# Performance work log

Hardware: AMD Instinct MI355X
Metric: run time of the kernel (lower is better)

## Reference

```python
import jax, jax.numpy as jnp
import numpy as np

D_MODEL = 1024
D_INNER = 2048  # d_model * expand_factor
EPS = 1e-6


def setup_inputs() -> dict:
    key = jax.random.key(0)
    ks = jax.random.split(key, 9)
    s_in = 1.0 / np.sqrt(D_MODEL)
    s_out = 1.0 / np.sqrt(D_INNER)
    x = jax.random.normal(ks[0], (4, 2048, D_MODEL), dtype=jnp.float32)
    # weights stored as [in, out] (transpose of nn.Linear layout)
    Wq = jax.random.uniform(ks[1], (D_MODEL, D_INNER), jnp.float32, -s_in, s_in)
    bq = jax.random.uniform(ks[2], (D_INNER,), jnp.float32, -s_in, s_in)
    Wk = jax.random.uniform(ks[3], (D_MODEL, D_INNER), jnp.float32, -s_in, s_in)
    bk = jax.random.uniform(ks[4], (D_INNER,), jnp.float32, -s_in, s_in)
    Wv = jax.random.uniform(ks[5], (D_MODEL, D_INNER), jnp.float32, -s_in, s_in)
    bv = jax.random.uniform(ks[6], (D_INNER,), jnp.float32, -s_in, s_in)
    Wo = jax.random.uniform(ks[7], (D_INNER, D_MODEL), jnp.float32, -s_out, s_out)
    bo = jax.random.uniform(ks[8], (D_MODEL,), jnp.float32, -s_out, s_out)
    return {"x": x, "Wq": Wq, "bq": bq, "Wk": Wk, "bk": bk,
            "Wv": Wv, "bv": bv, "Wo": Wo, "bo": bo}


def _phi(x):
    """ELU + 1 feature map (positive features)."""
    return jax.nn.elu(x) + 1.0


def reference(x, Wq, bq, Wk, bk, Wv, bv, Wo, bo):
    # x: [B, N, d_model]
    Q = _phi(x @ Wq + bq)          # [B, N, d_inner]
    K = _phi(x @ Wk + bk)          # [B, N, d_inner]
    V = x @ Wv + bv                # [B, N, d_inner]
    n = x.shape[1]
    # Causal linear attention; identical math to cumsum-of-outer-products:
    # numerator_n = sum_{m<=n} (Q_n . K_m) V_m ; denominator_n = sum_{m<=n} Q_n . K_m
    scores = jnp.einsum("bnd,bmd->bnm", Q, K)            # [B, N, N]
    mask = jnp.tril(jnp.ones((n, n), dtype=scores.dtype))
    scores = scores * mask
    numerator = jnp.einsum("bnm,bme->bne", scores, V)    # [B, N, d_inner]
    denominator = scores.sum(axis=-1, keepdims=True) + EPS
    out = numerator / denominator
    return out @ Wo + bo           # [B, N, d_model] (dropout is identity in eval)
```

## Files before the change

kernel.cpp:

```cpp
#include <hip/hip_runtime.h>
#include <hip/hip_bf16.h>


#define D_MODEL 1024
#define D_INNER 2048
#define SEQ     2048
#define NBATCH  4
#define MTOT    (NBATCH * SEQ)

typedef __attribute__((ext_vector_type(8))) __bf16 bf16x8;
typedef __attribute__((ext_vector_type(4))) float  f32x4;
typedef __attribute__((ext_vector_type(8))) short  short8v;
typedef __attribute__((ext_vector_type(4))) int    int4v;
typedef __attribute__((ext_vector_type(8))) int    int8v;

__device__ __forceinline__ short f2bf(float f) {
  union { float f; unsigned u; } x; x.f = f;
  unsigned r = x.u + 0x7fffu + ((x.u >> 16) & 1u);
  return (short)(r >> 16);
}
__device__ __forceinline__ float bf2f(short s) {
  union { unsigned u; float f; } x; x.u = ((unsigned)(unsigned short)s) << 16;
  return x.f;
}

__device__ __forceinline__ unsigned char f2fp8(float f) {
  union { float f; unsigned u; } x; x.f = f;
  const unsigned s = (x.u >> 24) & 0x80u;
  const unsigned a = x.u & 0x7fffffffu;
  if (a >= 0x43E00000u) return (unsigned char)(s | 0x7Eu);
  if (a < 0x3C800000u) {
    union { float f; unsigned u; } y; y.u = a;
    const int mi = (int)rintf(y.f * 512.0f);
    return (unsigned char)(s | (unsigned)mi);
  }
  const unsigned r = a + 0x7FFFFu + ((a >> 20) & 1u);
  const unsigned E = (r >> 23) - 120u;
  return (unsigned char)(s | (E << 3) | ((r >> 20) & 7u));
}

typedef const void __attribute__((address_space(1)))* as1cv;
typedef void __attribute__((address_space(3)))* as3v;

__device__ __forceinline__ void gload_lds16(const void* g, void* l) {
  __builtin_amdgcn_global_load_lds((as1cv)g, (as3v)l, 16, 0, 0);
}

__device__ __forceinline__ f32x4 mfma16(bf16x8 a, bf16x8 b, f32x4 c) {
  return __builtin_amdgcn_mfma_f32_16x16x32_bf16(a, b, c, 0, 0, 0);
}

__device__ __forceinline__ f32x4 mfma_fp8(int8v a, int8v b, f32x4 c) {
  asm("v_mfma_f32_16x16x128_f8f6f4 %0, %1, %2, %0"
      : "+v"(c) : "v"(a), "v"(b));
  return c;
}

__device__ __forceinline__ void gemm_pipe(const short* __restrict__ A, int lda, int aRowBase,
                                          const short* __restrict__ B, int ldb, int bRowBase,
                                          int k0, int k1, short* smem, f32x4 acc[4][4]) {
  const int t    = threadIdx.x;
  const int lane = t & 63, wid = t >> 6;
  const int wr = wid >> 1, wc = wid & 1;
  const int lrow = lane & 15, kblk = lane >> 4;

  const int r0 = t >> 2;
  const int sc = ((t & 3) ^ ((t >> 3) & 3)) * 8;
  const short* pA = A + (size_t)(aRowBase + r0) * lda + (k0 + sc);
  const short* pB = B + (size_t)(bRowBase + r0) * ldb + (k0 + sc);
  const size_t rA = (size_t)64 * lda;
  const size_t rB = (size_t)64 * ldb;

  int aoff[4], boff[4];
#pragma unroll
  for (int m = 0; m < 4; ++m) {
    const int row = wr * 64 + m * 16 + lrow;
    aoff[m] = (row * 64 + kblk * 16) ^ (((row >> 1) & 3) << 4);
  }
#pragma unroll
  for (int n = 0; n < 4; ++n) {
    const int row = wc * 64 + n * 16 + lrow;
    boff[n] = (row * 64 + kblk * 16) ^ (((row >> 1) & 3) << 4);
  }
  const char* cs = (const char*)smem;

#define STG(bufShorts) do {                                                    \
    gload_lds16(pA, smem + (bufShorts) + t * 8);                               \
    gload_lds16(pA + rA, smem + (bufShorts) + 2048 + t * 8);                   \
    gload_lds16(pB, smem + (bufShorts) + 4096 + t * 8);                        \
    gload_lds16(pB + rB, smem + (bufShorts) + 6144 + t * 8);                   \
    pA += 32; pB += 32;                                                        \
  } while (0)

#define CSTEP(bufBytes) do {                                                   \
    bf16x8 a[4], b[4];                                                         \
    _Pragma("unroll") for (int m = 0; m < 4; ++m)                              \
      a[m] = *(const bf16x8*)(cs + (bufBytes) + aoff[m]);                      \
    _Pragma("unroll") for (int n = 0; n < 4; ++n)                              \
      b[n] = *(const bf16x8*)(cs + (bufBytes) + 8192 + boff[n]);               \
    _Pragma("unroll") for (int m = 0; m < 4; ++m)                              \
      _Pragma("unroll") for (int n = 0; n < 4; ++n)                            \
        acc[m][n] = mfma16(a[m], b[n], acc[m][n]);                             \
  } while (0)

  STG(0);
  __syncthreads();
  for (int k = k0; k < k1; k += 64) {
    if (k + 32 < k1) STG(8192);
    CSTEP(0);
    __syncthreads();
    if (k + 64 < k1) STG(0);
    CSTEP(16384);
    __syncthreads();
  }
#undef STG
#undef CSTEP
}

__device__ __forceinline__ void gemm_pipe8(const unsigned char* __restrict__ A, int lda, int aRowBase,
                                           const unsigned char* __restrict__ B, int ldb, int bRowBase,
                                           int k0, int k1, char* smem, f32x4 acc[4][4]) {
  const int t    = threadIdx.x;
  const int lane = t & 63, wid = t >> 6;
  const int wr = wid >> 1, wc = wid & 1;
  const int lrow = lane & 15, kblk = lane >> 4;

  const int srow = t >> 3;
  const int scol = (((t & 7) ^ ((t >> 3) & 7)) << 4);
  const unsigned char* pA = A + (size_t)(aRowBase + srow) * lda + (k0 + scol);
  const unsigned char* pB = B + (size_t)(bRowBase + srow) * ldb + (k0 + scol);

  int aoff[4][2], boff[4][2];
#pragma unroll
  for (int m = 0; m < 4; ++m) {
    const int row = wr * 64 + m * 16 + lrow;
#pragma unroll
    for (int j = 0; j < 2; ++j)
      aoff[m][j] = row * 128 + (((kblk * 2 + j) ^ (row & 7)) << 4);
  }
#pragma unroll
  for (int n = 0; n < 4; ++n) {
    const int row = wc * 64 + n * 16 + lrow;
#pragma unroll
    for (int j = 0; j < 2; ++j)
      boff[n][j] = row * 128 + (((kblk * 2 + j) ^ (row & 7)) << 4);
  }

#define STG8(bufB) do {                                                        \
    _Pragma("unroll") for (int i = 0; i < 4; ++i) {                            \
      gload_lds16(pA + (size_t)(32 * i) * lda, smem + (bufB) + i * 4096 + t * 16);      \
      gload_lds16(pB + (size_t)(32 * i) * ldb, smem + (bufB) + 16384 + i * 4096 + t * 16); \
    }                                                                          \
    pA += 128; pB += 128;                                                      \
  } while (0)

#define CSTEP8(bufB) do {                                                      \
    int8v a[4], b[4];                                                          \
    _Pragma("unroll") for (int m = 0; m < 4; ++m)                              \
      _Pragma("unroll") for (int j = 0; j < 2; ++j)                            \
        ((int4v*)&a[m])[j] = *(const int4v*)(smem + (bufB) + aoff[m][j]);      \
    _Pragma("unroll") for (int n = 0; n < 4; ++n)                              \
      _Pragma("unroll") for (int j = 0; j < 2; ++j)                            \
        ((int4v*)&b[n])[j] = *(const int4v*)(smem + (bufB) + 16384 + boff[n][j]); \
    _Pragma("unroll") for (int m = 0; m < 4; ++m)                              \
      _Pragma("unroll") for (int n = 0; n < 4; ++n)                            \
        acc[m][n] = mfma_fp8(a[m], b[n], acc[m][n]);                           \
  } while (0)

  STG8(0);
  __syncthreads();
  for (int k = k0; k < k1; k += 256) {
    if (k + 128 < k1) STG8(32768);
    CSTEP8(0);
    __syncthreads();
    if (k + 256 < k1) STG8(0);
    CSTEP8(32768);
    __syncthreads();
  }
#undef STG8
#undef CSTEP8
}

#define GEMM_PRE                                           \
  __shared__ __align__(16) short smem[4 * 4096];           \
  f32x4 acc[4][4];                                         \
  _Pragma("unroll")                                        \
  for (int m = 0; m < 4; ++m)                              \
    _Pragma("unroll")                                      \
    for (int n = 0; n < 4; ++n) acc[m][n] = (f32x4){0.f, 0.f, 0.f, 0.f};

#define GEMM_PRE8                                          \
  __shared__ __align__(16) char smem8[65536];              \
  f32x4 acc[4][4];                                         \
  _Pragma("unroll")                                        \
  for (int m = 0; m < 4; ++m)                              \
    _Pragma("unroll")                                      \
    for (int n = 0; n < 4; ++n) acc[m][n] = (f32x4){0.f, 0.f, 0.f, 0.f};

#define EPILOG_VARS                                        \
  const int lane = threadIdx.x & 63;                       \
  const int wid  = threadIdx.x >> 6;                       \
  const int wr = wid >> 1, wc = wid & 1;                   \
  const int lrow = lane & 15, kblk = lane >> 4;

__global__ __launch_bounds__(256) void k_proj_qk8(const unsigned char* __restrict__ X8,
                                                  const unsigned char* __restrict__ WT8,
                                                  const float* __restrict__ bq,
                                                  const float* __restrict__ bk,
                                                  unsigned char* __restrict__ Qm8,
                                                  unsigned char* __restrict__ Km8) {
  GEMM_PRE8
  const int blockM = blockIdx.y * 128;
  const int blockN = blockIdx.x * 128;
  gemm_pipe8(X8, D_MODEL, blockM, WT8, D_MODEL, blockN, 0, D_MODEL, smem8, acc);
  EPILOG_VARS
  const int seg = blockN >> 11;
  const float* bias = (seg == 0) ? bq : bk;
  unsigned char* dst = (seg == 0) ? Qm8 : Km8;
#pragma unroll
  for (int m = 0; m < 4; ++m)
#pragma unroll
    for (int n = 0; n < 4; ++n) {
      const int e = (blockN & 2047) + wc * 64 + n * 16 + lrow;
      const float bvv = bias[e];
#pragma unroll
      for (int j = 0; j < 4; ++j) {
        const int row = blockM + wr * 64 + m * 16 + kblk * 4 + j;
        float v = acc[m][n][j] + bvv;
        v = (v > 0.f) ? (v + 1.f) : __expf(v);
        dst[(size_t)row * D_INNER + e] = f2fp8(v);
      }
    }
}

__global__ __launch_bounds__(256) void k_proj_v(const short* __restrict__ X,
                                                const short* __restrict__ WvT,
                                                const float* __restrict__ bv,
                                                short* __restrict__ V) {
  GEMM_PRE
  const int blockM = blockIdx.y * 128;
  const int blockN = blockIdx.x * 128;
  gemm_pipe(X, D_MODEL, blockM, WvT, D_MODEL, blockN, 0, D_MODEL, smem, acc);
  EPILOG_VARS
#pragma unroll
  for (int m = 0; m < 4; ++m)
#pragma unroll
    for (int n = 0; n < 4; ++n) {
      const int e = blockN + wc * 64 + n * 16 + lrow;
      const float bvv = bv[e];
#pragma unroll
      for (int j = 0; j < 4; ++j) {
        const int row = blockM + wr * 64 + m * 16 + kblk * 4 + j;
        V[(size_t)row * D_INNER + e] = f2bf(acc[m][n][j] + bvv);
      }
    }
}

__global__ __launch_bounds__(256) void k_vw(const short* __restrict__ V,
                                            const short* __restrict__ WoT,
                                            short* __restrict__ w2T) {
  GEMM_PRE
  const int blockM = blockIdx.y * 128;
  const int blockN = blockIdx.x * 128;
  gemm_pipe(V, D_INNER, blockM, WoT, D_INNER, blockN, 0, D_INNER, smem, acc);
  EPILOG_VARS
#pragma unroll
  for (int m = 0; m < 4; ++m)
#pragma unroll
    for (int n = 0; n < 4; ++n) {
      const int cl = wc * 64 + n * 16 + lrow;
#pragma unroll
      for (int j = 0; j < 4; ++j) {
        const int rl = wr * 64 + m * 16 + kblk * 4 + j;
        int byte = cl * 256 + rl * 2;
        byte ^= (cl & 7) << 5;
        *(short*)((char*)smem + byte) = f2bf(acc[m][n][j]);
      }
    }
  __syncthreads();
  const int b   = blockM >> 11;
  const int mm0 = blockM & 2047;
  const int er  = threadIdx.x >> 1;
  const int hf  = threadIdx.x & 1;
  short* dst = w2T + ((size_t)b * D_MODEL + blockN + er) * SEQ + mm0 + hf * 64;
#pragma unroll
  for (int i = 0; i < 8; ++i) {
    int byte = er * 256 + hf * 128 + i * 16;
    byte ^= (er & 7) << 5;
    ((short8v*)dst)[i] = *(const short8v*)((const char*)smem + byte);
  }
}

__global__ __launch_bounds__(256) void k_qkt8(const unsigned char* __restrict__ Q8,
                                              const unsigned char* __restrict__ K8,
                                              short* __restrict__ S,
                                              float* __restrict__ den_part) {
  const int b = blockIdx.y;
  const int t = blockIdx.x;
  int ib = (int)((-1.0f + sqrtf(8.0f * (float)t + 1.0f)) * 0.5f);
  while ((ib + 1) * (ib + 2) / 2 <= t) ++ib;
  while (ib * (ib + 1) / 2 > t) --ib;
  const int jb = t - ib * (ib + 1) / 2;
  GEMM_PRE8
  short* Sb = S + (size_t)b * SEQ * SEQ;
  gemm_pipe8(Q8 + (size_t)b * SEQ * D_INNER, D_INNER, ib * 128,
             K8 + (size_t)b * SEQ * D_INNER, D_INNER, jb * 128,
             0, D_INNER, smem8, acc);
  EPILOG_VARS
  const bool diag = (jb == ib);
  float sums[4][4];
#pragma unroll
  for (int m = 0; m < 4; ++m)
#pragma unroll
    for (int j = 0; j < 4; ++j) sums[m][j] = 0.f;
#pragma unroll
  for (int m = 0; m < 4; ++m)
#pragma unroll
    for (int n = 0; n < 4; ++n) {
      const int col = jb * 128 + wc * 64 + n * 16 + lrow;
#pragma unroll
      for (int j = 0; j < 4; ++j) {
        const int row = ib * 128 + wr * 64 + m * 16 + kblk * 4 + j;
        float v = acc[m][n][j];
        if (diag && col > row) v = 0.f;
        const short bs = f2bf(v);
        Sb[(size_t)row * SEQ + col] = bs;
        sums[m][j] += bf2f(bs);
      }
    }
#pragma unroll
  for (int m = 0; m < 4; ++m)
#pragma unroll
    for (int j = 0; j < 4; ++j) {
      float red = sums[m][j];
      red += __shfl_xor(red, 1, 64);
      red += __shfl_xor(red, 2, 64);
      red += __shfl_xor(red, 4, 64);
      red += __shfl_xor(red, 8, 64);
      if (lrow == 0) {
        const int rloc = wr * 64 + m * 16 + kblk * 4 + j;
        den_part[(size_t)(2 * jb + wc) * MTOT + b * SEQ + ib * 128 + rloc] = red;
      }
    }
}

__global__ __launch_bounds__(256) void k_sv(const short* __restrict__ S,
                                            const short* __restrict__ W2T,
                                            const float* __restrict__ den_part,
                                            const float* __restrict__ bo,
                                            float* __restrict__ out) {
  const int b = blockIdx.z;
  const int ib = 15 - blockIdx.y;
  const int eb = blockIdx.x;
  __shared__ float dnm[128];
  {
    const int t = threadIdx.x;
    if (t < 128) {
      float s = 1e-6f;
      const int nv = 2 * (ib + 1);
      const float* dp = den_part + b * SEQ + ib * 128 + t;
      for (int q = 0; q < nv; ++q) s += dp[(size_t)q * MTOT];
      dnm[t] = 1.0f / s;
    }
  }
  GEMM_PRE
  gemm_pipe(S + (size_t)b * SEQ * SEQ, SEQ, ib * 128,
            W2T + (size_t)b * (size_t)D_MODEL * SEQ, SEQ, eb * 128,
            0, (ib + 1) * 128, smem, acc);
  EPILOG_VARS
  const int blockM = ib * 128;
#pragma unroll
  for (int m = 0; m < 4; ++m)
#pragma unroll
    for (int j = 0; j < 4; ++j) {
      const int rloc = wr * 64 + m * 16 + kblk * 4 + j;
      const int row = blockM + rloc;
      const float rcp = dnm[rloc];
#pragma unroll
      for (int n = 0; n < 4; ++n) {
        const int col = eb * 128 + wc * 64 + n * 16 + lrow;
        out[((size_t)(b * SEQ + row)) * D_MODEL + col] = acc[m][n][j] * rcp + bo[col];
      }
    }
}

__global__ void k_cvt(const float* __restrict__ in, short* __restrict__ outb,
                      unsigned char* __restrict__ out8, int n4) {
  int i = blockIdx.x * blockDim.x + threadIdx.x;
  const int stride = gridDim.x * blockDim.x;
  for (; i < n4; i += stride) {
    float4 v = ((const float4*)in)[i];
    short4 o;
    o.x = f2bf(v.x); o.y = f2bf(v.y); o.z = f2bf(v.z); o.w = f2bf(v.w);
    ((short4*)outb)[i] = o;
    uchar4 q;
    q.x = f2fp8(v.x); q.y = f2fp8(v.y); q.z = f2fp8(v.z); q.w = f2fp8(v.w);
    ((uchar4*)out8)[i] = q;
  }
}

__global__ __launch_bounds__(256) void k_transposeAll(const float* __restrict__ w0,
                                                      const float* __restrict__ w1,
                                                      const float* __restrict__ w2,
                                                      const float* __restrict__ w3,
                                                      unsigned char* __restrict__ wqkT8,
                                                      short* __restrict__ wvT,
                                                      short* __restrict__ woT) {
  __shared__ float tl[32][33];
  const int z = blockIdx.z;
  const float* in = (z == 0) ? w0 : (z == 1) ? w1 : (z == 2) ? w2 : w3;
  const int R = (z < 3) ? 1024 : 2048;
  const int C = (z < 3) ? 2048 : 1024;
  const int nbx = C >> 5;
  const int c0 = (blockIdx.x % nbx) * 32, r0 = (blockIdx.x / nbx) * 32;
  const int tx = threadIdx.x & 31, ty = (threadIdx.x >> 5) * 4;
#pragma unroll
  for (int i = 0; i < 4; ++i)
    tl[ty + i][tx] = in[(size_t)(r0 + ty + i) * C + (c0 + tx)];
  __syncthreads();
  if (z < 2) {
    unsigned char* o = wqkT8 + (size_t)z * D_INNER * D_MODEL;
#pragma unroll
    for (int i = 0; i < 4; ++i)
      o[(size_t)(c0 + ty + i) * R + (r0 + tx)] = f2fp8(tl[tx][ty + i]);
  } else {
    short* o = (z == 2) ? wvT : woT;
#pragma unroll
    for (int i = 0; i < 4; ++i)
      o[(size_t)(c0 + ty + i) * R + (r0 + tx)] = f2bf(tl[tx][ty + i]);
  }
}

extern "C" void kernel_launch(void* const* d_in, const int* in_sizes, int n_in,
                              void* d_out, int out_size, void* d_ws, size_t ws_size,
                              hipStream_t stream) {
  const float* x  = (const float*)d_in[0];
  const float* Wq = (const float*)d_in[1];
  const float* bq = (const float*)d_in[2];
  const float* Wk = (const float*)d_in[3];
  const float* bk = (const float*)d_in[4];
  const float* Wv = (const float*)d_in[5];
  const float* bv = (const float*)d_in[6];
  const float* Wo = (const float*)d_in[7];
  const float* bo = (const float*)d_in[8];
  float* out = (float*)d_out;

  short* xb    = (short*)d_ws;
  short* wvT   = xb    + (size_t)MTOT * D_MODEL;
  short* woT   = wvT   + (size_t)D_INNER * D_MODEL;
  short* V     = woT   + (size_t)D_MODEL * D_INNER;
  short* Sc    = V     + (size_t)MTOT * D_INNER;
  short* w2T   = Sc    + (size_t)NBATCH * SEQ * SEQ;
  unsigned char* x8    = (unsigned char*)(w2T + (size_t)NBATCH * D_MODEL * SEQ);
  unsigned char* wqkT8 = x8    + (size_t)MTOT * D_MODEL;
  unsigned char* Qm8   = wqkT8 + (size_t)2 * D_INNER * D_MODEL;
  unsigned char* Km8   = Qm8   + (size_t)MTOT * D_INNER;
  float* den_part      = (float*)(Km8 + (size_t)MTOT * D_INNER);

  dim3 b256(256);
  k_cvt<<<2048, b256, 0, stream>>>(x, xb, x8, MTOT * D_MODEL / 4);
  k_transposeAll<<<dim3(2048, 1, 4), b256, 0, stream>>>(Wq, Wk, Wv, Wo, wqkT8, wvT, woT);

  k_proj_qk8<<<dim3(32, 64), b256, 0, stream>>>(x8, wqkT8, bq, bk, Qm8, Km8);
  k_proj_v  <<<dim3(16, 64), b256, 0, stream>>>(xb, wvT, bv, V);

  k_qkt8<<<dim3(136, NBATCH), b256, 0, stream>>>(Qm8, Km8, Sc, den_part);
  k_vw  <<<dim3(8, 64), b256, 0, stream>>>(V, woT, w2T);
  k_sv  <<<dim3(8, 16, NBATCH), b256, 0, stream>>>(Sc, w2T, den_part, bo, out);
}
```

Baseline: 284.5 us.

## Fold Wv and Wo into one fused weight before the value projection

Precomputes Wf = Wv·Wo (1024x1024) and a fused bias bv·Wo, so (xWv+bv)Wo becomes x·Wf + bf. This replaces the x→V projection (8192x2048x1024) and the V→Wo GEMM (8192x1024x2048) with one 8192x1024x1024 GEMM plus a small weight GEMM. It removes the V intermediate and its memory traffic. The cost is extra weight preprocessing on every call, including a naive serial bias reduction kernel, and slightly different bf16 rounding.

```diff
diff --git a/kernel.cpp b/kernel.cpp
--- a/kernel.cpp
+++ b/kernel.cpp
@@ -202,6 +202,18 @@
   const int wid  = threadIdx.x >> 6;                       \
   const int wr = wid >> 1, wc = wid & 1;                   \
   const int lrow = lane & 15, kblk = lane >> 4;
+
+__device__ __forceinline__ void retile_store(const short* smem, short* dst0, int ldd) {
+  const int er  = threadIdx.x >> 1;
+  const int hf  = threadIdx.x & 1;
+  short* dst = dst0 + (size_t)er * ldd + hf * 64;
+#pragma unroll
+  for (int i = 0; i < 8; ++i) {
+    int byte = er * 256 + hf * 128 + i * 16;
+    byte ^= (er & 7) << 5;
+    ((short8v*)dst)[i] = *(const short8v*)((const char*)smem + byte);
+  }
+}
 
 __global__ __launch_bounds__(256) void k_proj_qk8(const unsigned char* __restrict__ X8,
                                                   const unsigned char* __restrict__ WT8,
@@ -233,36 +245,13 @@
     }
 }
 
-__global__ __launch_bounds__(256) void k_proj_v(const short* __restrict__ X,
-                                                const short* __restrict__ WvT,
-                                                const float* __restrict__ bv,
-                                                short* __restrict__ V) {
+__global__ __launch_bounds__(256) void k_wfuse(const short* __restrict__ WvB,
+                                               const short* __restrict__ WoT,
+                                               short* __restrict__ wfT) {
   GEMM_PRE
   const int blockM = blockIdx.y * 128;
   const int blockN = blockIdx.x * 128;
-  gemm_pipe(X, D_MODEL, blockM, WvT, D_MODEL, blockN, 0, D_MODEL, smem, acc);
-  EPILOG_VARS
-#pragma unroll
-  for (int m = 0; m < 4; ++m)
-#pragma unroll
-    for (int n = 0; n < 4; ++n) {
-      const int e = blockN + wc * 64 + n * 16 + lrow;
-      const float bvv = bv[e];
-#pragma unroll
-      for (int j = 0; j < 4; ++j) {
-        const int row = blockM + wr * 64 + m * 16 + kblk * 4 + j;
-        V[(size_t)row * D_INNER + e] = f2bf(acc[m][n][j] + bvv);
-      }
-    }
-}
-
-__global__ __launch_bounds__(256) void k_vw(const short* __restrict__ V,
-                                            const short* __restrict__ WoT,
-                                            short* __restrict__ w2T) {
-  GEMM_PRE
-  const int blockM = blockIdx.y * 128;
-  const int blockN = blockIdx.x * 128;
-  gemm_pipe(V, D_INNER, blockM, WoT, D_INNER, blockN, 0, D_INNER, smem, acc);
+  gemm_pipe(WvB, D_INNER, blockM, WoT, D_INNER, blockN, 0, D_INNER, smem, acc);
   EPILOG_VARS
 #pragma unroll
   for (int m = 0; m < 4; ++m)
@@ -278,17 +267,46 @@
       }
     }
   __syncthreads();
+  retile_store(smem, wfT + (size_t)blockN * D_MODEL + blockM, D_MODEL);
+}
+
+__global__ __launch_bounds__(256) void k_bfuse(const float* __restrict__ bv,
+                                               const float* __restrict__ Wo,
+                                               float* __restrict__ bfuse) {
+  const int o = blockIdx.x * 256 + threadIdx.x;
+  float s = 0.f;
+  for (int e = 0; e < D_INNER; ++e)
+    s += bv[e] * Wo[(size_t)e * D_MODEL + o];
+  bfuse[o] = s;
+}
+
+__global__ __launch_bounds__(256) void k_w2(const short* __restrict__ X,
+                                            const short* __restrict__ WfT,
+                                            const float* __restrict__ bfuse,
+                                            short* __restrict__ w2T) {
+  GEMM_PRE
+  const int blockM = blockIdx.y * 128;
+  const int blockN = blockIdx.x * 128;
+  gemm_pipe(X, D_MODEL, blockM, WfT, D_MODEL, blockN, 0, D_MODEL, smem, acc);
+  EPILOG_VARS
+#pragma unroll
+  for (int m = 0; m < 4; ++m)
+#pragma unroll
+    for (int n = 0; n < 4; ++n) {
+      const int cl = wc * 64 + n * 16 + lrow;
+      const float bvv = bfuse[blockN + cl];
+#pragma unroll
+      for (int j = 0; j < 4; ++j) {
+        const int rl = wr * 64 + m * 16 + kblk * 4 + j;
+        int byte = cl * 256 + rl * 2;
+        byte ^= (cl & 7) << 5;
+        *(short*)((char*)smem + byte) = f2bf(acc[m][n][j] + bvv);
+      }
+    }
+  __syncthreads();
   const int b   = blockM >> 11;
   const int mm0 = blockM & 2047;
-  const int er  = threadIdx.x >> 1;
-  const int hf  = threadIdx.x & 1;
-  short* dst = w2T + ((size_t)b * D_MODEL + blockN + er) * SEQ + mm0 + hf * 64;
-#pragma unroll
-  for (int i = 0; i < 8; ++i) {
-    int byte = er * 256 + hf * 128 + i * 16;
-    byte ^= (er & 7) << 5;
-    ((short8v*)dst)[i] = *(const short8v*)((const char*)smem + byte);
-  }
+  retile_store(smem, w2T + ((size_t)b * D_MODEL + blockN) * SEQ + mm0, SEQ);
 }
 
 __global__ __launch_bounds__(256) void k_qkt8(const unsigned char* __restrict__ Q8,
@@ -404,7 +422,7 @@
                                                       const float* __restrict__ w2,
                                                       const float* __restrict__ w3,
                                                       unsigned char* __restrict__ wqkT8,
-                                                      short* __restrict__ wvT,
+                                                      short* __restrict__ wvB,
                                                       short* __restrict__ woT) {
   __shared__ float tl[32][33];
   const int z = blockIdx.z;
@@ -414,6 +432,14 @@
   const int nbx = C >> 5;
   const int c0 = (blockIdx.x % nbx) * 32, r0 = (blockIdx.x / nbx) * 32;
   const int tx = threadIdx.x & 31, ty = (threadIdx.x >> 5) * 4;
+  if (z == 2) {
+#pragma unroll
+    for (int i = 0; i < 4; ++i) {
+      const size_t idx = (size_t)(r0 + ty + i) * C + (c0 + tx);
+      wvB[idx] = f2bf(in[idx]);
+    }
+    return;
+  }
 #pragma unroll
   for (int i = 0; i < 4; ++i)
     tl[ty + i][tx] = in[(size_t)(r0 + ty + i) * C + (c0 + tx)];
@@ -424,10 +450,9 @@
     for (int i = 0; i < 4; ++i)
       o[(size_t)(c0 + ty + i) * R + (r0 + tx)] = f2fp8(tl[tx][ty + i]);
   } else {
-    short* o = (z == 2) ? wvT : woT;
 #pragma unroll
     for (int i = 0; i < 4; ++i)
-      o[(size_t)(c0 + ty + i) * R + (r0 + tx)] = f2bf(tl[tx][ty + i]);
+      woT[(size_t)(c0 + ty + i) * R + (r0 + tx)] = f2bf(tl[tx][ty + i]);
   }
 }
 
@@ -446,25 +471,28 @@
   float* out = (float*)d_out;
 
   short* xb    = (short*)d_ws;
-  short* wvT   = xb    + (size_t)MTOT * D_MODEL;
-  short* woT   = wvT   + (size_t)D_INNER * D_MODEL;
-  short* V     = woT   + (size_t)D_MODEL * D_INNER;
-  short* Sc    = V     + (size_t)MTOT * D_INNER;
+  short* wvB   = xb    + (size_t)MTOT * D_MODEL;
+  short* woT   = wvB   + (size_t)D_MODEL * D_INNER;
+  short* wfT   = woT   + (size_t)D_MODEL * D_INNER;
+  short* Sc    = wfT   + (size_t)D_MODEL * D_MODEL;
   short* w2T   = Sc    + (size_t)NBATCH * SEQ * SEQ;
   unsigned char* x8    = (unsigned char*)(w2T + (size_t)NBATCH * D_MODEL * SEQ);
   unsigned char* wqkT8 = x8    + (size_t)MTOT * D_MODEL;
   unsigned char* Qm8   = wqkT8 + (size_t)2 * D_INNER * D_MODEL;
   unsigned char* Km8   = Qm8   + (size_t)MTOT * D_INNER;
   float* den_part      = (float*)(Km8 + (size_t)MTOT * D_INNER);
+  float* bfuse         = den_part + (size_t)32 * MTOT;
 
   dim3 b256(256);
   k_cvt<<<2048, b256, 0, stream>>>(x, xb, x8, MTOT * D_MODEL / 4);
-  k_transposeAll<<<dim3(2048, 1, 4), b256, 0, stream>>>(Wq, Wk, Wv, Wo, wqkT8, wvT, woT);
+  k_transposeAll<<<dim3(2048, 1, 4), b256, 0, stream>>>(Wq, Wk, Wv, Wo, wqkT8, wvB, woT);
+
+  k_bfuse<<<4, b256, 0, stream>>>(bv, Wo, bfuse);
+  k_wfuse<<<dim3(8, 8), b256, 0, stream>>>(wvB, woT, wfT);
 
   k_proj_qk8<<<dim3(32, 64), b256, 0, stream>>>(x8, wqkT8, bq, bk, Qm8, Km8);
-  k_proj_v  <<<dim3(16, 64), b256, 0, stream>>>(xb, wvT, bv, V);
-
   k_qkt8<<<dim3(136, NBATCH), b256, 0, stream>>>(Qm8, Km8, Sc, den_part);
-  k_vw  <<<dim3(8, 64), b256, 0, stream>>>(V, woT, w2T);
-  k_sv  <<<dim3(8, 16, NBATCH), b256, 0, stream>>>(Sc, w2T, den_part, bo, out);
-}
+
+  k_w2<<<dim3(8, 64), b256, 0, stream>>>(xb, wfT, bfuse, w2T);
+  k_sv<<<dim3(8, 16, NBATCH), b256, 0, stream>>>(Sc, w2T, den_part, bo, out);
+}
```

Measured after the change: 305.4 us. 1.07x slower.
